# Kernel optimization log

Hardware: AMD Instinct MI355X
Metric: run time of the kernel (lower is better)

The kernel has to match this reference:

```python
import jax, jax.numpy as jnp
import numpy as np

B, L, F = 8, 2048, 4
DM, DI, N, DCONV, DTRANK = 320, 1280, 16, 8, 20  # d_model, d_inner, d_state, d_conv, dt_rank
NBLK = 4


def setup_inputs() -> dict:
    key = jax.random.key(0)
    ks = jax.random.split(key, 24)
    s = 0.05
    inp = {
        "x": jax.random.uniform(ks[0], (B, L, F), jnp.float32),
        "fc_w": jax.random.normal(ks[1], (320, 4), jnp.float32) * s,
        "fc_b": jnp.zeros((320,), jnp.float32),
        "blk_lin_w": jax.random.normal(ks[2], (NBLK, 320, 320), jnp.float32) * s,
        "blk_lin_b": jnp.zeros((NBLK, 320), jnp.float32),
        "blk_inproj_w": jax.random.normal(ks[3], (NBLK, 2 * DI, DM), jnp.float32) * s,
        "blk_conv_w": jax.random.normal(ks[4], (NBLK, DI, DCONV), jnp.float32) * s,
        "blk_conv_b": jnp.zeros((NBLK, DI), jnp.float32),
        "blk_xproj_w": jax.random.normal(ks[5], (NBLK, DTRANK + 2 * N, DI), jnp.float32) * s,
        "blk_dtproj_w": jax.random.normal(ks[6], (NBLK, DI, DTRANK), jnp.float32) * s,
        "blk_dtproj_b": jnp.full((NBLK, DI), -4.0, jnp.float32),  # softplus(-4) ~ 0.018, stable dt
        "blk_A_log": jnp.tile(jnp.log(jnp.arange(1, N + 1, dtype=jnp.float32)), (NBLK, DI, 1)),
        "blk_D": jnp.ones((NBLK, DI), jnp.float32),
        "blk_outproj_w": jax.random.normal(ks[7], (NBLK, DM, DI), jnp.float32) * s,
        "s1_w1": jax.random.normal(ks[8], (512, 320), jnp.float32) * s,
        "s1_b1": jnp.zeros((512,), jnp.float32),
        "s1_w2": jax.random.normal(ks[9], (512, 512), jnp.float32) * s,
        "s1_b2": jnp.zeros((512,), jnp.float32),
        "s1_w3": jax.random.normal(ks[10], (1, 512), jnp.float32) * s,
        "s1_b3": jnp.zeros((1,), jnp.float32),
    }
    return inp


def _mamba(u, inproj_w, conv_w, conv_b, xproj_w, dtproj_w, dtproj_b, A_log, D):
    # u: (B, L, DM)
    xz = u @ inproj_w.T                       # (B, L, 2*DI)
    x, z = jnp.split(xz, 2, axis=-1)
    # causal depthwise conv1d over time
    xc = jnp.transpose(x, (0, 2, 1))          # (B, DI, L)
    xc = jax.lax.conv_general_dilated(
        xc, conv_w[:, None, :], (1,), [(DCONV - 1, 0)],
        feature_group_count=DI, dimension_numbers=("NCH", "OIH", "NCH"))
    xc = xc + conv_b[None, :, None]
    x = jax.nn.silu(jnp.transpose(xc, (0, 2, 1)))  # (B, L, DI)
    dbc = x @ xproj_w.T                        # (B, L, DTRANK + 2N)
    dt, Bm, Cm = jnp.split(dbc, [DTRANK, DTRANK + N], axis=-1)
    delta = jax.nn.softplus(dt @ dtproj_w.T + dtproj_b)  # (B, L, DI)
    A = -jnp.exp(A_log)                        # (DI, N)

    def step(h, inp):
        xt, dt_t, Bt, Ct = inp                 # (B,DI),(B,DI),(B,N),(B,N)
        dA = jnp.exp(dt_t[..., None] * A)      # (B, DI, N)
        h = dA * h + (dt_t * xt)[..., None] * Bt[:, None, :]
        y = jnp.einsum("bdn,bn->bd", h, Ct)
        return h, y

    h0 = jnp.zeros((u.shape[0], DI, N), x.dtype)
    xs = (jnp.swapaxes(x, 0, 1), jnp.swapaxes(delta, 0, 1),
          jnp.swapaxes(Bm, 0, 1), jnp.swapaxes(Cm, 0, 1))
    _, ys = jax.lax.scan(step, h0, xs)         # ys: (L, B, DI)
    y = jnp.swapaxes(ys, 0, 1) + x * D         # (B, L, DI)
    y = y * jax.nn.silu(z)
    return y


def reference(x, fc_w, fc_b, blk_lin_w, blk_lin_b, blk_inproj_w, blk_conv_w,
              blk_conv_b, blk_xproj_w, blk_dtproj_w, blk_dtproj_b, blk_A_log,
              blk_D, blk_outproj_w, s1_w1, s1_b1, s1_w2, s1_b2, s1_w3, s1_b3):
    seq_len = x.shape[1]
    start_max = jnp.max(x[:, :, 2])
    xn = jnp.stack([x[:, :, 0] / 255.0,
                    x[:, :, 1] / 255.0,
                    x[:, :, 2] / start_max,
                    x[:, :, 3]], axis=-1)
    out = xn @ fc_w.T + fc_b                   # (B, L, 320)
    for i in range(NBLK):
        out = jnp.tanh(out @ blk_lin_w[i].T + blk_lin_b[i])
        out = _mamba(out, blk_inproj_w[i], blk_conv_w[i], blk_conv_b[i],
                     blk_xproj_w[i], blk_dtproj_w[i], blk_dtproj_b[i],
                     blk_A_log[i], blk_D[i]) @ blk_outproj_w[i].T
        out = jax.nn.elu(out)                  # dropout p=1e-6 -> identity (eval)
    h = out[:, -1, :]                          # (B, 320)
    h = jax.nn.relu(h @ s1_w1.T + s1_b1)
    h = jax.nn.relu(h @ s1_w2.T + s1_b2)
    h = h @ s1_w3.T + s1_b3                    # (B, 1)
    scale = start_max / (1.0 + np.log(seq_len))
    h = h.at[:, 0].multiply(scale)
    return jax.nn.relu(h)
```

## Files before the change

kernel.cpp:

```cpp
#include <hip/hip_runtime.h>
#include <math.h>

#define BSZ 8
#define LSZ 2048
#define DMV 320
#define DIV 1280
#define NST 16
#define DCV 8
#define DTR 20
#define NBLKV 4
#define MTOT (BSZ*LSZ)
#define NCHUNK 32
#define CLEN 64
#define DBLD 56

typedef __attribute__((ext_vector_type(8))) short short8;
typedef __attribute__((ext_vector_type(8))) unsigned short ushort8;
typedef __attribute__((ext_vector_type(4))) float floatx4;

__device__ inline unsigned short f2bf(float f) {
    union { float f; unsigned u; } v; v.f = f;
    unsigned r = v.u + 0x7FFFu + ((v.u >> 16) & 1u);
    return (unsigned short)(r >> 16);
}
__device__ inline float bf2f(unsigned short b) {
    union { unsigned u; float f; } v; v.u = ((unsigned)b) << 16;
    return v.f;
}

__device__ __forceinline__ void gload_lds16(unsigned short* l, const unsigned short* g) {
    __builtin_amdgcn_global_load_lds(
        (const __attribute__((address_space(1))) unsigned int*)g,
        (__attribute__((address_space(3))) unsigned int*)l, 16, 0, 0);
}

__global__ __launch_bounds__(256) void convert_kernel(
    const float* __restrict__ src, unsigned short* __restrict__ dst, long n4) {
    long i = (long)blockIdx.x * 256 + threadIdx.x;
    if (i >= n4) return;
    float4 v = *(const float4*)(src + i * 4);
    unsigned short o[4] = {f2bf(v.x), f2bf(v.y), f2bf(v.z), f2bf(v.w)};
    *(unsigned long long*)(dst + i * 4) = *(unsigned long long*)o;
}

__global__ __launch_bounds__(256) void convert_dtw_kernel(
    const float* __restrict__ src, unsigned short* __restrict__ dst) {
    int i = blockIdx.x * 256 + threadIdx.x;
    if (i >= NBLKV * DIV * 32) return;
    int l = i / (DIV * 32), rem = i % (DIV * 32);
    int d = rem >> 5, j = rem & 31;
    dst[i] = (j < DTR) ? f2bf(src[((long)l * DIV + d) * DTR + j]) : (unsigned short)0;
}

__global__ __launch_bounds__(256) void convert_xp_kernel(
    const float* __restrict__ src, unsigned short* __restrict__ dst) {
    int i = blockIdx.x * 256 + threadIdx.x;
    if (i >= NBLKV * 64 * DIV) return;
    int l = i / (64 * DIV), rem = i % (64 * DIV);
    int n = rem / DIV, k = rem % DIV;
    dst[i] = (n < DTR + 2 * NST) ? f2bf(src[((long)l * (DTR + 2 * NST) + n) * DIV + k])
                                 : (unsigned short)0;
}

__global__ __launch_bounds__(256) void convert_t2_kernel(
    const float* __restrict__ src, unsigned short* __restrict__ dst, int N, int K) {
    int i = blockIdx.x * 256 + threadIdx.x;
    if (i >= N * K) return;
    int n = i / K, k = i % K;
    dst[((k >> 1) * N + n) * 2 + (k & 1)] = f2bf(src[i]);
}

__global__ void init_sm_kernel(float* sm) {
    if (threadIdx.x == 0) ((int*)sm)[0] = 0;
}

__global__ void reduce_max_kernel(const float* __restrict__ x, float* sm) {
    int idx = blockIdx.x * blockDim.x + threadIdx.x;
    float v = 0.f;
    for (int i = idx; i < MTOT; i += gridDim.x * blockDim.x)
        v = fmaxf(v, x[i * 4 + 2]);
    #pragma unroll
    for (int off = 32; off > 0; off >>= 1)
        v = fmaxf(v, __shfl_xor(v, off, 64));
    if ((threadIdx.x & 63) == 0)
        atomicMax((int*)sm, __float_as_int(v));
}

__global__ __launch_bounds__(256) void fc_kernel(
    const float* __restrict__ x, const float* __restrict__ fw,
    const float* __restrict__ fb, const float* __restrict__ sm,
    unsigned short* __restrict__ u) {
    int o = blockIdx.x * 64 + (threadIdx.x & 63);
    long m = (long)blockIdx.y * 4 + (threadIdx.x >> 6);
    float inv_sm = 1.0f / sm[0];
    float x0 = x[m * 4 + 0] * (1.0f / 255.0f);
    float x1 = x[m * 4 + 1] * (1.0f / 255.0f);
    float x2 = x[m * 4 + 2] * inv_sm;
    float x3 = x[m * 4 + 3];
    float acc = fb[o];
    acc = fmaf(x0, fw[o * 4 + 0], acc);
    acc = fmaf(x1, fw[o * 4 + 1], acc);
    acc = fmaf(x2, fw[o * 4 + 2], acc);
    acc = fmaf(x3, fw[o * 4 + 3], acc);
    u[m * DMV + o] = f2bf(acc);
}

template<int ACT, int BM, int BN, int KB, typename TOUT>
__global__ __launch_bounds__(256) void gemm_mfma_kernel(
    const unsigned short* __restrict__ X, const unsigned short* __restrict__ W,
    const float* __restrict__ bias, TOUT* __restrict__ Y,
    int N, int K, long ldx, long ldy)
{
    constexpr int WMT = (BM == 128 && BN == 128) ? 4 : 2;
    constexpr int WNT = (BM == 64 && BN == 64) ? 2 : 4;
    constexpr int CPR = KB / 8;
    constexpr int NCX = BM * CPR / 256;
    constexpr int NCW = BN * CPR / 256;
    __shared__ unsigned short Xs[BM * KB];
    __shared__ unsigned short Ws[BN * KB];

    int tid = threadIdx.x;
    int wave = tid >> 6, lane = tid & 63;
    int quad = lane >> 4, l15 = lane & 15;
    int wmbase, wnbase;
    if (BM == 128 && BN == 128)      { wmbase = (wave & 1) * 64; wnbase = (wave >> 1) * 64; }
    else if (BM == 128 && BN == 64)  { wmbase = wave * 32;       wnbase = 0; }
    else                             { wmbase = (wave & 1) * 32; wnbase = (wave >> 1) * 32; }
    long m0 = (long)blockIdx.y * BM;
    int n0 = blockIdx.x * BN;

    floatx4 acc[WMT][WNT];
    #pragma unroll
    for (int i = 0; i < WMT; i++)
        #pragma unroll
        for (int j = 0; j < WNT; j++)
            acc[i][j] = (floatx4){0.f, 0.f, 0.f, 0.f};

    const unsigned short* Xb = X + m0 * ldx;
    const unsigned short* Wb = W + (long)n0 * K;

    for (int k0 = 0; k0 < K; k0 += KB) {
        #pragma unroll
        for (int j = 0; j < NCX; j++) {
            int s = (wave * NCX + j) * 64 + lane;
            int r = s / CPR, c = s % CPR;
            gload_lds16(&Xs[(wave * NCX + j) * 512],
                        Xb + (long)r * ldx + k0 + c * 8);
        }
        #pragma unroll
        for (int j = 0; j < NCW; j++) {
            int s = (wave * NCW + j) * 64 + lane;
            int r = s / CPR, c = s % CPR;
            gload_lds16(&Ws[(wave * NCW + j) * 512],
                        Wb + (long)r * K + k0 + c * 8);
        }
        __syncthreads();
        #pragma unroll
        for (int kk = 0; kk < KB; kk += 32) {
            short8 af[WMT], bfr[WNT];
            #pragma unroll
            for (int i = 0; i < WMT; i++)
                af[i] = *(short8*)&Xs[(wmbase + i * 16 + l15) * KB + kk + quad * 8];
            #pragma unroll
            for (int j = 0; j < WNT; j++)
                bfr[j] = *(short8*)&Ws[(wnbase + j * 16 + l15) * KB + kk + quad * 8];
            #pragma unroll
            for (int i = 0; i < WMT; i++)
                #pragma unroll
                for (int j = 0; j < WNT; j++)
                    acc[i][j] = __builtin_amdgcn_mfma_f32_16x16x32_bf16(
                        af[i], bfr[j], acc[i][j], 0, 0, 0);
        }
        __syncthreads();
    }

    #pragma unroll
    for (int i = 0; i < WMT; i++) {
        long mb = m0 + wmbase + i * 16 + quad * 4;
        #pragma unroll
        for (int j = 0; j < WNT; j++) {
            int n = n0 + wnbase + j * 16 + l15;
            if (n >= N) continue;
            float bv = bias ? bias[n] : 0.f;
            #pragma unroll
            for (int r = 0; r < 4; r++) {
                float v = acc[i][j][r] + bv;
                if (ACT == 1) v = tanhf(v);
                else if (ACT == 3) v = (v > 0.f) ? v : expm1f(v);
                else if (ACT == 4) v = (v > 20.f) ? v : __logf(1.0f + __expf(v));
                if constexpr (sizeof(TOUT) == 2)
                    Y[(mb + r) * ldy + n] = f2bf(v);
                else
                    Y[(mb + r) * ldy + n] = v;
            }
        }
    }
}

__global__ __launch_bounds__(512) void head_kernel(
    const unsigned short* __restrict__ u,
    const unsigned short* __restrict__ w1t, const float* __restrict__ b1,
    const unsigned short* __restrict__ w2t, const float* __restrict__ b2,
    const float* __restrict__ w3, const float* __restrict__ b3,
    const float* __restrict__ sm, float* __restrict__ out)
{
    __shared__ float xs[DMV];
    __shared__ float h1s[512];
    __shared__ float red[8];
    int b = blockIdx.x;
    int tid = threadIdx.x;
    const unsigned short* xr = u + ((long)b * LSZ + (LSZ - 1)) * DMV;
    if (tid < DMV) xs[tid] = bf2f(xr[tid]);
    __syncthreads();

    float acc = 0.f;
    #pragma unroll 8
    for (int kk = 0; kk < DMV / 2; kk++) {
        unsigned wv = *(const unsigned*)&w1t[((long)kk * 512 + tid) * 2];
        acc = fmaf(xs[2 * kk],     bf2f((unsigned short)(wv & 0xffffu)), acc);
        acc = fmaf(xs[2 * kk + 1], bf2f((unsigned short)(wv >> 16)), acc);
    }
    h1s[tid] = fmaxf(acc + b1[tid], 0.f);
    __syncthreads();

    acc = 0.f;
    #pragma unroll 8
    for (int kk = 0; kk < 256; kk++) {
        unsigned wv = *(const unsigned*)&w2t[((long)kk * 512 + tid) * 2];
        acc = fmaf(h1s[2 * kk],     bf2f((unsigned short)(wv & 0xffffu)), acc);
        acc = fmaf(h1s[2 * kk + 1], bf2f((unsigned short)(wv >> 16)), acc);
    }
    float h2 = fmaxf(acc + b2[tid], 0.f);

    float part = h2 * w3[tid];
    #pragma unroll
    for (int off = 32; off > 0; off >>= 1) part += __shfl_xor(part, off, 64);
    if ((tid & 63) == 0) red[tid >> 6] = part;
    __syncthreads();
    if (tid == 0) {
        float s = b3[0];
        #pragma unroll
        for (int w = 0; w < 8; w++) s += red[w];
        float scale = sm[0] / 8.624618986159398f;
        out[b] = fmaxf(s * scale, 0.f);
    }
}

#define TCONV 32
__global__ __launch_bounds__(256) void conv_kernel(
    const unsigned short* __restrict__ xz, const float* __restrict__ cw,
    const float* __restrict__ cb, unsigned short* __restrict__ xc)
{
    int d = blockIdx.x * 256 + threadIdx.x;
    int lb = blockIdx.z;
    int l0 = blockIdx.y * TCONV;
    long base = (long)lb * LSZ + l0;

    float w[8];
    #pragma unroll
    for (int k = 0; k < 8; k++) w[k] = cw[d * 8 + k];
    float bc = cb[d];

    float win[8];
    #pragma unroll
    for (int i = 0; i < 7; i++) {
        int l = l0 - 7 + i;
        win[i] = (l >= 0) ? bf2f(xz[(base - 7 + i) * 2560 + d]) : 0.f;
    }
    #pragma unroll
    for (int s = 0; s < TCONV; s++) {
        win[7] = bf2f(xz[(base + s) * 2560 + d]);
        float acc = bc;
        #pragma unroll
        for (int k = 0; k < 8; k++) acc = fmaf(win[k], w[k], acc);
        float sv = acc / (1.0f + __expf(-acc));
        xc[(base + s) * DIV + d] = f2bf(sv);
        #pragma unroll
        for (int k = 0; k < 7; k++) win[k] = win[k + 1];
    }
}

__device__ inline void pow_ladder(float p, float* pw) {
    pw[0] = p;
    pw[1] = pw[0] * pw[0];
    pw[2] = pw[1] * pw[0];
    pw[3] = pw[1] * pw[1];
    pw[4] = pw[3] * pw[0];
    pw[5] = pw[3] * pw[1];
    pw[6] = pw[3] * pw[2];
    pw[7] = pw[3] * pw[3];
    #pragma unroll
    for (int k = 8; k < 16; k++) pw[k] = pw[7] * pw[k - 8];
}

__global__ __launch_bounds__(256) void scan_local_kernel(
    const unsigned short* __restrict__ xc, unsigned short* xz,
    const unsigned short* __restrict__ dbc, const unsigned short* __restrict__ delta,
    const float* __restrict__ A_log, const float* __restrict__ Dp,
    float* __restrict__ hfin, float* __restrict__ sumd)
{
    __shared__ float S[CLEN * 32];
    int lb = blockIdx.z;
    int ch = blockIdx.y;
    int d = blockIdx.x * 256 + threadIdx.x;
    int tid = threadIdx.x;

    float a[NST], h[NST];
    #pragma unroll
    for (int n = 0; n < NST; n++) {
        a[n] = -__expf(A_log[d * NST + n]);
        h[n] = 0.f;
    }
    float a0 = a[0];
    bool geo = true;
    #pragma unroll
    for (int n = 1; n < NST; n++)
        geo = geo && (fabsf(a[n] - (float)(n + 1) * a0) <= 1e-4f * (float)(n + 1));
    float Dd = Dp[d];

    long tok0 = (long)lb * LSZ + ch * CLEN;
    for (int i = tid; i < CLEN * 32; i += 256) {
        int r = i >> 5, c = i & 31;
        S[i] = bf2f(dbc[(tok0 + r) * DBLD + 20 + c]);
    }
    __syncthreads();

    float sd = 0.f;
    if (__all(geo)) {
        for (int l = 0; l < CLEN; l++) {
            long m = tok0 + l;
            const float* row = &S[l * 32];
            float dl = bf2f(delta[m * DIV + d]);
            sd += dl;
            float xv = bf2f(xc[m * DIV + d]);
            float db = dl * xv;
            float pw[NST];
            pow_ladder(__expf(dl * a0), pw);
            float y = 0.f;
            #pragma unroll
            for (int n = 0; n < NST; n++) {
                h[n] = fmaf(pw[n], h[n], db * row[n]);
                y = fmaf(h[n], row[16 + n], y);
            }
            y = fmaf(xv, Dd, y);
            xz[m * 2560 + d] = f2bf(y);
        }
    } else {
        for (int l = 0; l < CLEN; l++) {
            long m = tok0 + l;
            const float* row = &S[l * 32];
            float dl = bf2f(delta[m * DIV + d]);
            sd += dl;
            float xv = bf2f(xc[m * DIV + d]);
            float db = dl * xv;
            float y = 0.f;
            #pragma unroll
            for (int n = 0; n < NST; n++) {
                float dA = __expf(dl * a[n]);
                h[n] = fmaf(dA, h[n], db * row[n]);
                y = fmaf(h[n], row[16 + n], y);
            }
            y = fmaf(xv, Dd, y);
            xz[m * 2560 + d] = f2bf(y);
        }
    }

    long cidx = ((long)lb * NCHUNK + ch) * DIV + d;
    #pragma unroll
    for (int n = 0; n < NST; n++) hfin[cidx * NST + n] = h[n];
    sumd[cidx] = sd;
}

__global__ __launch_bounds__(256) void scan_prefix_kernel(
    float* __restrict__ hfin, const float* __restrict__ sumd,
    const float* __restrict__ A_log, int Bc)
{
    long g = (long)blockIdx.x * 256 + threadIdx.x;
    int n = (int)(g & (NST - 1));
    long t = g >> 4;
    int d = (int)(t % DIV);
    int lb = (int)(t / DIV);
    if (lb >= Bc) return;

    float a = -__expf(A_log[d * NST + n]);
    float s = 0.f;
    for (int c = 0; c < NCHUNK; c++) {
        long cidx = ((long)lb * NCHUNK + c) * DIV + d;
        float hl = hfin[cidx * NST + n];
        float P = __expf(a * sumd[cidx]);
        hfin[cidx * NST + n] = s;
        s = fmaf(P, s, hl);
    }
}

__global__ __launch_bounds__(256) void scan_fix_kernel(
    unsigned short* xz, const unsigned short* __restrict__ dbc,
    const unsigned short* __restrict__ delta,
    const float* __restrict__ A_log, const float* __restrict__ hfin)
{
    __shared__ float S[CLEN * 16];
    int lb = blockIdx.z;
    int ch = blockIdx.y;
    int d = blockIdx.x * 256 + threadIdx.x;
    int tid = threadIdx.x;

    float a[NST], hr[NST];
    #pragma unroll
    for (int n = 0; n < NST; n++) a[n] = -__expf(A_log[d * NST + n]);
    float a0 = a[0];
    bool geo = true;
    #pragma unroll
    for (int n = 1; n < NST; n++)
        geo = geo && (fabsf(a[n] - (float)(n + 1) * a0) <= 1e-4f * (float)(n + 1));

    long cidx = ((long)lb * NCHUNK + ch) * DIV + d;
    #pragma unroll
    for (int n = 0; n < NST; n += 4)
        *(float4*)&hr[n] = *(const float4*)&hfin[cidx * NST + n];

    long tok0 = (long)lb * LSZ + ch * CLEN;
    for (int i = tid; i < CLEN * 16; i += 256) {
        int r = i >> 4, c = i & 15;
        S[i] = bf2f(dbc[(tok0 + r) * DBLD + 36 + c]);
    }
    __syncthreads();

    if (__all(geo)) {
        for (int l = 0; l < CLEN; l++) {
            long m = tok0 + l;
            const float* row = &S[l * 16];
            float dl = bf2f(delta[m * DIV + d]);
            float pw[NST];
            pow_ladder(__expf(dl * a0), pw);
            float fix = 0.f;
            #pragma unroll
            for (int n = 0; n < NST; n++) {
                hr[n] *= pw[n];
                fix = fmaf(hr[n], row[n], fix);
            }
            float y = bf2f(xz[m * 2560 + d]) + fix;
            float zv = bf2f(xz[m * 2560 + 1280 + d]);
            float sz = zv / (1.0f + __expf(-zv));
            xz[m * 2560 + d] = f2bf(y * sz);
        }
    } else {
        for (int l = 0; l < CLEN; l++) {
            long m = tok0 + l;
            const float* row = &S[l * 16];
            float dl = bf2f(delta[m * DIV + d]);
            float fix = 0.f;
            #pragma unroll
            for (int n = 0; n < NST; n++) {
                hr[n] *= __expf(dl * a[n]);
                fix = fmaf(hr[n], row[n], fix);
            }
            float y = bf2f(xz[m * 2560 + d]) + fix;
            float zv = bf2f(xz[m * 2560 + 1280 + d]);
            float sz = zv / (1.0f + __expf(-zv));
            xz[m * 2560 + d] = f2bf(y * sz);
        }
    }
}

extern "C" void kernel_launch(void* const* d_in, const int* in_sizes, int n_in,
                              void* d_out, int out_size, void* d_ws, size_t ws_size,
                              hipStream_t stream) {
    const float* x        = (const float*)d_in[0];
    const float* fc_w     = (const float*)d_in[1];
    const float* fc_b     = (const float*)d_in[2];
    const float* lin_w    = (const float*)d_in[3];
    const float* lin_b    = (const float*)d_in[4];
    const float* inproj_w = (const float*)d_in[5];
    const float* conv_w   = (const float*)d_in[6];
    const float* conv_b   = (const float*)d_in[7];
    const float* xproj_w  = (const float*)d_in[8];
    const float* dtproj_w = (const float*)d_in[9];
    const float* dtproj_b = (const float*)d_in[10];
    const float* A_log    = (const float*)d_in[11];
    const float* Dp       = (const float*)d_in[12];
    const float* outproj_w= (const float*)d_in[13];
    const float* s1_w1    = (const float*)d_in[14];
    const float* s1_b1    = (const float*)d_in[15];
    const float* s1_w2    = (const float*)d_in[16];
    const float* s1_b2    = (const float*)d_in[17];
    const float* s1_w3    = (const float*)d_in[18];
    const float* s1_b3    = (const float*)d_in[19];

    const long NLIN = (long)NBLKV * DMV * DMV;
    const long NINP = (long)NBLKV * 2 * DIV * DMV;
    const long NXPP = (long)NBLKV * 64 * DIV;
    const long NOUT = (long)NBLKV * DMV * DIV;
    const long NDTW = (long)NBLKV * DIV * 32;
    const long NHW1 = (long)512 * DMV;
    const long NHW2 = (long)512 * 512;

    const long FIXED = 256 +
                       (NLIN + NINP + NXPP + NOUT + NDTW + NHW1 + NHW2) * 2 + 256;
    const long PER_BATCH = (long)LSZ * (DMV + DMV + 2 * DIV + DIV) * 2
                         + (long)LSZ * DBLD * 2
                         + (long)LSZ * DIV * 2
                         + (long)NCHUNK * DIV * NST * 4
                         + (long)NCHUNK * DIV * 4;
    int Bc = 8;
    while (Bc > 1 && (size_t)(FIXED + (long)Bc * PER_BATCH) > ws_size)
        Bc >>= 1;
    int nchunk_b = BSZ / Bc;
    long Mc = (long)Bc * LSZ;

    char* p = (char*)d_ws;
    float* sm = (float*)p;           p += 256;
    unsigned short* wlin = (unsigned short*)p; p += NLIN * 2;
    unsigned short* winp = (unsigned short*)p; p += NINP * 2;
    unsigned short* wxp  = (unsigned short*)p; p += NXPP * 2;
    unsigned short* wout = (unsigned short*)p; p += NOUT * 2;
    unsigned short* wdt  = (unsigned short*)p; p += NDTW * 2;
    unsigned short* w1t  = (unsigned short*)p; p += NHW1 * 2;
    unsigned short* w2t  = (unsigned short*)p; p += NHW2 * 2;
    unsigned short* u  = (unsigned short*)p;   p += Mc * DMV * 2;
    unsigned short* t  = (unsigned short*)p;   p += Mc * DMV * 2;
    unsigned short* xz = (unsigned short*)p;   p += Mc * 2560 * 2;
    unsigned short* xc = (unsigned short*)p;   p += Mc * DIV * 2;
    unsigned short* dbc = (unsigned short*)p;  p += Mc * DBLD * 2;
    unsigned short* delta = (unsigned short*)p; p += Mc * DIV * 2;
    float* hfin = (float*)p;         p += (long)Bc * NCHUNK * DIV * NST * 4;
    float* sumd = (float*)p;

    convert_kernel<<<(unsigned)((NLIN / 4 + 255) / 256), 256, 0, stream>>>(lin_w, wlin, NLIN / 4);
    convert_kernel<<<(unsigned)((NINP / 4 + 255) / 256), 256, 0, stream>>>(inproj_w, winp, NINP / 4);
    convert_kernel<<<(unsigned)((NOUT / 4 + 255) / 256), 256, 0, stream>>>(outproj_w, wout, NOUT / 4);
    convert_xp_kernel<<<(unsigned)((NXPP + 255) / 256), 256, 0, stream>>>(xproj_w, wxp);
    convert_dtw_kernel<<<(unsigned)((NDTW + 255) / 256), 256, 0, stream>>>(dtproj_w, wdt);
    convert_t2_kernel<<<(unsigned)((NHW1 + 255) / 256), 256, 0, stream>>>(s1_w1, w1t, 512, DMV);
    convert_t2_kernel<<<(unsigned)((NHW2 + 255) / 256), 256, 0, stream>>>(s1_w2, w2t, 512, 512);

    init_sm_kernel<<<1, 64, 0, stream>>>(sm);
    reduce_max_kernel<<<32, 256, 0, stream>>>(x, sm);

    for (int c = 0; c < nchunk_b; c++) {
        int b0 = c * Bc;
        fc_kernel<<<dim3(5, (unsigned)(Mc / 4)), 256, 0, stream>>>(
            x + (long)b0 * LSZ * 4, fc_w, fc_b, sm, u);

        for (int i = 0; i < NBLKV; i++) {
            const float* lb  = lin_b    + (long)i * DMV;
            const float* cw  = conv_w   + (long)i * DIV * DCV;
            const float* cb  = conv_b   + (long)i * DIV;
            const float* dpb = dtproj_b + (long)i * DIV;
            const float* al  = A_log    + (long)i * DIV * NST;
            const float* dd  = Dp       + (long)i * DIV;

            gemm_mfma_kernel<1, 128, 64, 64, unsigned short>
                <<<dim3(5, (unsigned)(Mc / 128)), 256, 0, stream>>>(
                u, wlin + (long)i * DMV * DMV, lb, t, DMV, DMV, DMV, DMV);
            gemm_mfma_kernel<0, 128, 128, 64, unsigned short>
                <<<dim3(20, (unsigned)(Mc / 128)), 256, 0, stream>>>(
                t, winp + (long)i * 2 * DIV * DMV, nullptr, xz, 2 * DIV, DMV, DMV, 2 * DIV);
            conv_kernel<<<dim3(5, LSZ / TCONV, Bc), 256, 0, stream>>>(xz, cw, cb, xc);
            gemm_mfma_kernel<0, 64, 64, 64, unsigned short>
                <<<dim3(1, (unsigned)(Mc / 64)), 256, 0, stream>>>(
                xc, wxp + (long)i * 64 * DIV, nullptr, dbc,
                DTR + 2 * NST, DIV, DIV, DBLD);
            gemm_mfma_kernel<4, 128, 128, 32, unsigned short>
                <<<dim3(10, (unsigned)(Mc / 128)), 256, 0, stream>>>(
                dbc, wdt + (long)i * DIV * 32, dpb, delta, DIV, 32, DBLD, DIV);
            scan_local_kernel<<<dim3(5, NCHUNK, Bc), 256, 0, stream>>>(
                xc, xz, dbc, delta, al, dd, hfin, sumd);
            scan_prefix_kernel<<<dim3(Bc * 80), 256, 0, stream>>>(hfin, sumd, al, Bc);
            scan_fix_kernel<<<dim3(5, NCHUNK, Bc), 256, 0, stream>>>(
                xz, dbc, delta, al, hfin);
            gemm_mfma_kernel<3, 128, 64, 64, unsigned short>
                <<<dim3(5, (unsigned)(Mc / 128)), 256, 0, stream>>>(
                xz, wout + (long)i * DMV * DIV, nullptr, u, DMV, DIV, 2 * DIV, DMV);
        }

        head_kernel<<<Bc, 512, 0, stream>>>(u, w1t, s1_b1, w2t, s1_b2,
                                            s1_w3, s1_b3, sm, (float*)d_out + b0);
    }
}
```

Before: 1.381 ms.

## Swizzle GEMM LDS tiles and use cumulative delta in scan fix pass

The GEMM kernel now XOR-swizzles the 16-byte chunk column by row, both when loading global data into LDS and when reading MFMA fragments, to reduce LDS bank conflicts. The local scan kernel overwrites delta with its running in-chunk cumulative sum. The fix kernel then computes the carried-in state's decay directly as exp(a*cumsum) instead of a serial per-step multiply chain. This removes a loop-carried dependency in the fix pass but adds a store per step in the local scan, and storing the cumulative sum in bf16 loses precision for later tokens.

```diff
diff --git a/kernel.cpp b/kernel.cpp
--- a/kernel.cpp
+++ b/kernel.cpp
@@ -114,6 +114,7 @@
     constexpr int WMT = (BM == 128 && BN == 128) ? 4 : 2;
     constexpr int WNT = (BM == 64 && BN == 64) ? 2 : 4;
     constexpr int CPR = KB / 8;
+    constexpr int CMSK = CPR - 1;
     constexpr int NCX = BM * CPR / 256;
     constexpr int NCW = BN * CPR / 256;
     __shared__ unsigned short Xs[BM * KB];
@@ -144,26 +145,34 @@
         for (int j = 0; j < NCX; j++) {
             int s = (wave * NCX + j) * 64 + lane;
             int r = s / CPR, c = s % CPR;
+            int cg = c ^ (r & CMSK);
             gload_lds16(&Xs[(wave * NCX + j) * 512],
-                        Xb + (long)r * ldx + k0 + c * 8);
+                        Xb + (long)r * ldx + k0 + cg * 8);
         }
         #pragma unroll
         for (int j = 0; j < NCW; j++) {
             int s = (wave * NCW + j) * 64 + lane;
             int r = s / CPR, c = s % CPR;
+            int cg = c ^ (r & CMSK);
             gload_lds16(&Ws[(wave * NCW + j) * 512],
-                        Wb + (long)r * K + k0 + c * 8);
+                        Wb + (long)r * K + k0 + cg * 8);
         }
         __syncthreads();
         #pragma unroll
         for (int kk = 0; kk < KB; kk += 32) {
             short8 af[WMT], bfr[WNT];
             #pragma unroll
-            for (int i = 0; i < WMT; i++)
-                af[i] = *(short8*)&Xs[(wmbase + i * 16 + l15) * KB + kk + quad * 8];
-            #pragma unroll
-            for (int j = 0; j < WNT; j++)
-                bfr[j] = *(short8*)&Ws[(wnbase + j * 16 + l15) * KB + kk + quad * 8];
+            for (int i = 0; i < WMT; i++) {
+                int R = wmbase + i * 16 + l15;
+                int cp = (kk / 8 + quad) ^ (R & CMSK);
+                af[i] = *(short8*)&Xs[R * KB + cp * 8];
+            }
+            #pragma unroll
+            for (int j = 0; j < WNT; j++) {
+                int R = wnbase + j * 16 + l15;
+                int cp = (kk / 8 + quad) ^ (R & CMSK);
+                bfr[j] = *(short8*)&Ws[R * KB + cp * 8];
+            }
             #pragma unroll
             for (int i = 0; i < WMT; i++)
                 #pragma unroll
@@ -295,7 +304,7 @@
 
 __global__ __launch_bounds__(256) void scan_local_kernel(
     const unsigned short* __restrict__ xc, unsigned short* xz,
-    const unsigned short* __restrict__ dbc, const unsigned short* __restrict__ delta,
+    const unsigned short* __restrict__ dbc, unsigned short* delta,
     const float* __restrict__ A_log, const float* __restrict__ Dp,
     float* __restrict__ hfin, float* __restrict__ sumd)
 {
@@ -332,6 +341,7 @@
             const float* row = &S[l * 32];
             float dl = bf2f(delta[m * DIV + d]);
             sd += dl;
+            delta[m * DIV + d] = f2bf(sd);
             float xv = bf2f(xc[m * DIV + d]);
             float db = dl * xv;
             float pw[NST];
@@ -351,6 +361,7 @@
             const float* row = &S[l * 32];
             float dl = bf2f(delta[m * DIV + d]);
             sd += dl;
+            delta[m * DIV + d] = f2bf(sd);
             float xv = bf2f(xc[m * DIV + d]);
             float db = dl * xv;
             float y = 0.f;
@@ -395,7 +406,7 @@
 
 __global__ __launch_bounds__(256) void scan_fix_kernel(
     unsigned short* xz, const unsigned short* __restrict__ dbc,
-    const unsigned short* __restrict__ delta,
+    const unsigned short* __restrict__ cum,
     const float* __restrict__ A_log, const float* __restrict__ hfin)
 {
     __shared__ float S[CLEN * 16];
@@ -404,7 +415,7 @@
     int d = blockIdx.x * 256 + threadIdx.x;
     int tid = threadIdx.x;
 
-    float a[NST], hr[NST];
+    float a[NST], hin[NST];
     #pragma unroll
     for (int n = 0; n < NST; n++) a[n] = -__expf(A_log[d * NST + n]);
     float a0 = a[0];
@@ -416,7 +427,7 @@
     long cidx = ((long)lb * NCHUNK + ch) * DIV + d;
     #pragma unroll
     for (int n = 0; n < NST; n += 4)
-        *(float4*)&hr[n] = *(const float4*)&hfin[cidx * NST + n];
+        *(float4*)&hin[n] = *(const float4*)&hfin[cidx * NST + n];
 
     long tok0 = (long)lb * LSZ + ch * CLEN;
     for (int i = tid; i < CLEN * 16; i += 256) {
@@ -429,15 +440,13 @@
         for (int l = 0; l < CLEN; l++) {
             long m = tok0 + l;
             const float* row = &S[l * 16];
-            float dl = bf2f(delta[m * DIV + d]);
+            float cm = bf2f(cum[m * DIV + d]);
             float pw[NST];
-            pow_ladder(__expf(dl * a0), pw);
+            pow_ladder(__expf(cm * a0), pw);
             float fix = 0.f;
             #pragma unroll
-            for (int n = 0; n < NST; n++) {
-                hr[n] *= pw[n];
-                fix = fmaf(hr[n], row[n], fix);
-            }
+            for (int n = 0; n < NST; n++)
+                fix = fmaf(hin[n] * pw[n], row[n], fix);
             float y = bf2f(xz[m * 2560 + d]) + fix;
             float zv = bf2f(xz[m * 2560 + 1280 + d]);
             float sz = zv / (1.0f + __expf(-zv));
@@ -447,13 +456,11 @@
         for (int l = 0; l < CLEN; l++) {
             long m = tok0 + l;
             const float* row = &S[l * 16];
-            float dl = bf2f(delta[m * DIV + d]);
+            float cm = bf2f(cum[m * DIV + d]);
             float fix = 0.f;
             #pragma unroll
-            for (int n = 0; n < NST; n++) {
-                hr[n] *= __expf(dl * a[n]);
-                fix = fmaf(hr[n], row[n], fix);
-            }
+            for (int n = 0; n < NST; n++)
+                fix = fmaf(hin[n] * __expf(cm * a[n]), row[n], fix);
             float y = bf2f(xz[m * 2560 + d]) + fix;
             float zv = bf2f(xz[m * 2560 + 1280 + d]);
             float sz = zv / (1.0f + __expf(-zv));
```

Result: faster. 1.275 ms (-7.7%).
